# Kernel tuning notes

Measured on AMD Instinct MI355X. Metric: run time of the kernel, lower is better.

The kernel has to match this reference:

```python
import jax, jax.numpy as jnp
import numpy as np

TMP = 1.0  # temperature from init

def setup_inputs() -> dict:
    key = jax.random.key(0)
    k1, k2, k3 = jax.random.split(key, 3)
    B, D, C = 8192, 1024, 4096
    x = jax.random.normal(k1, (B, D), dtype=jnp.float32)
    mod = jax.random.normal(k2, (B, D), dtype=jnp.float32)
    W = jax.random.normal(k3, (C, D), dtype=jnp.float32) * 0.02  # cls.weight
    return {"x": x, "mod": mod, "W": W}

def reference(x, mod, W):
    # att = softmax(mod / tmp, axis=1) + 1, shape (B, D)
    att = jax.nn.softmax(mod / TMP, axis=1) + 1.0
    # result[b, c] = sum_d W[c, d] * att[b, d] * x[b, d]
    # == (att * x) @ W.T  -- collapses the repeat + per-sample matvec loop
    return jnp.einsum('bd,cd->bc', att * x, W)
```

## Files before the change

### kernel.cpp

```cpp
#include <hip/hip_runtime.h>
#include <hip/hip_bf16.h>
#include <cstdint>
#include <cstddef>

typedef __bf16 bf16_t;
typedef __bf16 bf16x8 __attribute__((ext_vector_type(8)));
typedef __bf16 bf16x4 __attribute__((ext_vector_type(4)));
typedef float  f32x4  __attribute__((ext_vector_type(4)));

#define KDIM 1024
#define NT   16

__global__ void prep_kernel(const float* __restrict__ x,
                            const float* __restrict__ mod,
                            const float* __restrict__ W,
                            bf16_t* __restrict__ a,
                            bf16_t* __restrict__ Wb,
                            int D, int Bn) {
  if ((int)blockIdx.x >= Bn) {
    const size_t i = (((size_t)blockIdx.x - Bn) * blockDim.x + threadIdx.x) * 8;
    float4 u = *(const float4*)(W + i);
    float4 v = *(const float4*)(W + i + 4);
    bf16x8 o;
    o[0] = (bf16_t)u.x; o[1] = (bf16_t)u.y; o[2] = (bf16_t)u.z; o[3] = (bf16_t)u.w;
    o[4] = (bf16_t)v.x; o[5] = (bf16_t)v.y; o[6] = (bf16_t)v.z; o[7] = (bf16_t)v.w;
    *(bf16x8*)(Wb + i) = o;
    return;
  }

  const int b = blockIdx.x;
  const int t = threadIdx.x;
  const size_t row = (size_t)b * D;

  float4 mv = ((const float4*)(mod + row))[t];
  float mx = fmaxf(fmaxf(mv.x, mv.y), fmaxf(mv.z, mv.w));
#pragma unroll
  for (int o = 32; o > 0; o >>= 1) mx = fmaxf(mx, __shfl_xor(mx, o));

  __shared__ float redmax[4];
  __shared__ float redsum[4];
  const int wave = t >> 6, lane = t & 63;
  if (lane == 0) redmax[wave] = mx;
  __syncthreads();
  mx = fmaxf(fmaxf(redmax[0], redmax[1]), fmaxf(redmax[2], redmax[3]));

  float4 e;
  e.x = __expf(mv.x - mx); e.y = __expf(mv.y - mx);
  e.z = __expf(mv.z - mx); e.w = __expf(mv.w - mx);
  float s = (e.x + e.y) + (e.z + e.w);
#pragma unroll
  for (int o = 32; o > 0; o >>= 1) s += __shfl_xor(s, o);
  if (lane == 0) redsum[wave] = s;
  __syncthreads();
  s = (redsum[0] + redsum[1]) + (redsum[2] + redsum[3]);

  const float inv = 1.0f / s;
  float4 xv = ((const float4*)(x + row))[t];
  bf16x4 o4;
  o4[0] = (bf16_t)((e.x * inv + 1.0f) * xv.x);
  o4[1] = (bf16_t)((e.y * inv + 1.0f) * xv.y);
  o4[2] = (bf16_t)((e.z * inv + 1.0f) * xv.z);
  o4[3] = (bf16_t)((e.w * inv + 1.0f) * xv.w);
  *((bf16x4*)(a + row) + t) = o4;
}

__global__ __launch_bounds__(512, 2) void gemm256_kernel(
    const bf16_t* __restrict__ A, const bf16_t* __restrict__ B,
    float* __restrict__ C, int M, int N) {
  __shared__ __align__(16) bf16_t lds[2 * 32768];

  const int tid  = threadIdx.x;
  const int wave = tid >> 6;
  const int lane = tid & 63;
  const int quad = lane >> 4;
  const int l16  = lane & 15;
  const int wm   = wave >> 2;
  const int wn   = wave & 3;

  const int nwg = gridDim.x;
  int flat = blockIdx.x;
  flat = (flat & 7) * (nwg >> 3) + (flat >> 3);
  const int ntiles = N >> 8;
  const int m0 = (flat / ntiles) << 8;
  const int n0 = (flat % ntiles) << 8;

  const int trow = tid >> 3;
  const int colg = (tid & 7) ^ (trow & 7);
  const bf16_t* aSrc = A + (size_t)(m0 + trow) * KDIM + colg * 8;
  const bf16_t* bSrc = B + (size_t)(n0 + trow) * KDIM + colg * 8;
  const int ldsW = wave * 512;

#define GLDS(src_, dst_) __builtin_amdgcn_global_load_lds( \
      (const __attribute__((address_space(1))) void*)(src_), \
      (__attribute__((address_space(3))) void*)(dst_), 16, 0, 0)

#define ISSUE_A(h, t_) do { \
      const bf16_t* s_ = aSrc + (size_t)((h) * 128) * KDIM + (t_) * 64; \
      bf16_t* d_ = lds + ((t_) & 1) * 32768 + (h) * 8192 + ldsW; \
      GLDS(s_, d_); \
      GLDS(s_ + (size_t)64 * KDIM, d_ + 4096); \
    } while (0)

#define ISSUE_B(h, t_) do { \
      const bf16_t* s_ = bSrc + (size_t)((h) * 128) * KDIM + (t_) * 64; \
      bf16_t* d_ = lds + ((t_) & 1) * 32768 + 16384 + (h) * 8192 + ldsW; \
      GLDS(s_, d_); \
      GLDS(s_ + (size_t)64 * KDIM, d_ + 4096); \
    } while (0)

  ISSUE_A(0, 0); ISSUE_A(1, 0);
  ISSUE_B(0, 0); ISSUE_B(1, 0);
  ISSUE_B(0, 1); ISSUE_B(1, 1);

  f32x4 acc[8][4];
#pragma unroll
  for (int i = 0; i < 8; ++i)
#pragma unroll
    for (int j = 0; j < 4; ++j) acc[i][j] = (f32x4){0.f, 0.f, 0.f, 0.f};

  const int aBase = (wm * 128 + l16) * 64;
  const int bBase = (wn * 64 + l16) * 64;
  const int c0 = ((quad)     ^ (l16 & 7)) * 8;
  const int c1 = ((4 + quad) ^ (l16 & 7)) * 8;

  asm volatile("s_waitcnt vmcnt(4)" ::: "memory");
  __builtin_amdgcn_s_barrier();

  bf16x8 bfr[4][2];
  bf16x8 afA[2][2], afB[2][2];

#define BPANEL(Bt_) do { \
      _Pragma("unroll") \
      for (int j = 0; j < 4; ++j) { \
        bfr[j][0] = *(const bf16x8*)((Bt_) + bBase + j * 16 * 64 + c0); \
        bfr[j][1] = *(const bf16x8*)((Bt_) + bBase + j * 16 * 64 + c1); \
      } \
    } while (0)

#define RD_AF(S_, q_) do { \
      _Pragma("unroll") \
      for (int i = 0; i < 2; ++i) { \
        S_[i][0] = *(const bf16x8*)(At + aBase + ((q_) * 32 + i * 16) * 64 + c0); \
        S_[i][1] = *(const bf16x8*)(At + aBase + ((q_) * 32 + i * 16) * 64 + c1); \
      } \
    } while (0)

#define MFMA16(q_, S_) do { \
      _Pragma("unroll") \
      for (int i = 0; i < 2; ++i) \
        _Pragma("unroll") \
        for (int j = 0; j < 4; ++j) { \
          acc[(q_) * 2 + i][j] = __builtin_amdgcn_mfma_f32_16x16x32_bf16( \
              S_[i][0], bfr[j][0], acc[(q_) * 2 + i][j], 0, 0, 0); \
          acc[(q_) * 2 + i][j] = __builtin_amdgcn_mfma_f32_16x16x32_bf16( \
              S_[i][1], bfr[j][1], acc[(q_) * 2 + i][j], 0, 0, 0); \
        } \
    } while (0)

#define PH(qcur_, SCUR_, SNXT_, qnxt_, ISSUE_STMT, LGKM_STR, END_STMT) do { \
      if ((qnxt_) >= 0) { RD_AF(SNXT_, ((qnxt_) & 3)); } \
      ISSUE_STMT; \
      asm volatile("" ::: "memory"); \
      __builtin_amdgcn_s_barrier(); \
      asm volatile(LGKM_STR ::: "memory"); \
      __builtin_amdgcn_sched_barrier(0); \
      __builtin_amdgcn_s_setprio(1); \
      MFMA16(qcur_, SCUR_); \
      __builtin_amdgcn_s_setprio(0); \
      END_STMT; \
      asm volatile("" ::: "memory"); \
      __builtin_amdgcn_s_barrier(); \
    } while (0)

#pragma unroll 1
  for (int t = 0; t < NT; ++t) {
    const bf16_t* At = lds + (t & 1) * 32768;
    const bf16_t* Bt = At + 16384;

    BPANEL(Bt);
    RD_AF(afA, 0);

    PH(0, afA, afB, 1, if (t + 1 < NT) ISSUE_A(0, t + 1),
       "s_waitcnt lgkmcnt(4)", (void)0);
    PH(1, afB, afA, 2, if (t + 1 < NT) ISSUE_A(1, t + 1),
       "s_waitcnt lgkmcnt(4)", (void)0);
    PH(2, afA, afB, 3, if (t + 2 < NT) ISSUE_B(0, t + 2),
       "s_waitcnt lgkmcnt(4)", (void)0);
    PH(3, afB, afA, -1, if (t + 2 < NT) ISSUE_B(1, t + 2),
       "s_waitcnt lgkmcnt(0)",
       if (t < NT - 2) { asm volatile("s_waitcnt vmcnt(4)" ::: "memory"); }
       else            { asm volatile("s_waitcnt vmcnt(0)" ::: "memory"); });
  }

#pragma unroll
  for (int ri = 0; ri < 8; ++ri) {
    const int mg = m0 + wm * 128 + ri * 16 + quad * 4;
#pragma unroll
    for (int j = 0; j < 4; ++j) {
      const int ng = n0 + wn * 64 + j * 16 + l16;
#pragma unroll
      for (int r = 0; r < 4; ++r)
        C[(size_t)(mg + r) * N + ng] = acc[ri][j][r];
    }
  }
}

extern "C" void kernel_launch(void* const* d_in, const int* in_sizes, int n_in,
                              void* d_out, int out_size, void* d_ws, size_t ws_size,
                              hipStream_t stream) {
  const float* x   = (const float*)d_in[0];
  const float* mod = (const float*)d_in[1];
  const float* W   = (const float*)d_in[2];
  float* out = (float*)d_out;

  const int D = 1024;
  const int Bn = in_sizes[0] / D;
  const int Cn = in_sizes[2] / D;

  bf16_t* a  = (bf16_t*)d_ws;
  bf16_t* Wb = (bf16_t*)((char*)d_ws + (size_t)Bn * D * sizeof(bf16_t));

  const int castBlocks = (Cn * D) / (256 * 8);
  prep_kernel<<<Bn + castBlocks, 256, 0, stream>>>(x, mod, W, a, Wb, D, Bn);

  const int nwg = (Bn / 256) * (Cn / 256);
  gemm256_kernel<<<nwg, 512, 0, stream>>>(a, Wb, out, Bn, Cn);
}
```

Measured before the change: 256.2 us.

## Load B fragments directly from global into registers, keep only A in LDS

The GEMM stops staging B tiles through LDS. Each wave now loads its B fragments straight from global memory into double-buffered registers two K-tiles ahead, and only A goes through LDS via global_load_lds. The K loop is also restructured into a simpler per-tile schedule with one barrier per tile instead of the four-phase interleaved pipeline. This halves LDS traffic and footprint, at the cost of more VGPRs, uncoalesced per-lane global loads of B, and redundant B loads across the wm waves.

New measurement: 278.1 us. +8.5%, slower.

```diff
diff --git a/kernel.cpp b/kernel.cpp
--- a/kernel.cpp
+++ b/kernel.cpp
@@ -67,7 +67,7 @@
 __global__ __launch_bounds__(512, 2) void gemm256_kernel(
     const bf16_t* __restrict__ A, const bf16_t* __restrict__ B,
     float* __restrict__ C, int M, int N) {
-  __shared__ __align__(16) bf16_t lds[2 * 32768];
+  __shared__ __align__(16) bf16_t As[2][16384];
 
   const int tid  = threadIdx.x;
   const int wave = tid >> 6;
@@ -87,30 +87,36 @@
   const int trow = tid >> 3;
   const int colg = (tid & 7) ^ (trow & 7);
   const bf16_t* aSrc = A + (size_t)(m0 + trow) * KDIM + colg * 8;
-  const bf16_t* bSrc = B + (size_t)(n0 + trow) * KDIM + colg * 8;
   const int ldsW = wave * 512;
 
 #define GLDS(src_, dst_) __builtin_amdgcn_global_load_lds( \
       (const __attribute__((address_space(1))) void*)(src_), \
       (__attribute__((address_space(3))) void*)(dst_), 16, 0, 0)
 
-#define ISSUE_A(h, t_) do { \
-      const bf16_t* s_ = aSrc + (size_t)((h) * 128) * KDIM + (t_) * 64; \
-      bf16_t* d_ = lds + ((t_) & 1) * 32768 + (h) * 8192 + ldsW; \
-      GLDS(s_, d_); \
-      GLDS(s_ + (size_t)64 * KDIM, d_ + 4096); \
-    } while (0)
-
-#define ISSUE_B(h, t_) do { \
-      const bf16_t* s_ = bSrc + (size_t)((h) * 128) * KDIM + (t_) * 64; \
-      bf16_t* d_ = lds + ((t_) & 1) * 32768 + 16384 + (h) * 8192 + ldsW; \
-      GLDS(s_, d_); \
-      GLDS(s_ + (size_t)64 * KDIM, d_ + 4096); \
-    } while (0)
-
-  ISSUE_A(0, 0); ISSUE_A(1, 0);
-  ISSUE_B(0, 0); ISSUE_B(1, 0);
-  ISSUE_B(0, 1); ISSUE_B(1, 1);
+#define STAGE_A(t_) do { \
+      if ((t_) < NT) { \
+        _Pragma("unroll") \
+        for (int i_ = 0; i_ < 4; ++i_) { \
+          GLDS(aSrc + (size_t)(i_ * 64) * KDIM + (t_) * 64, \
+               &As[(t_) & 1][i_ * 4096 + ldsW]); \
+        } \
+      } \
+    } while (0)
+
+  const bf16_t* bP[4];
+#pragma unroll
+  for (int j = 0; j < 4; ++j)
+    bP[j] = B + (size_t)(n0 + wn * 64 + j * 16 + l16) * KDIM + quad * 8;
+
+#define PRELOAD_B(DST_, t_) do { \
+      if ((t_) < NT) { \
+        _Pragma("unroll") \
+        for (int j_ = 0; j_ < 4; ++j_) { \
+          DST_[j_][0] = *(const bf16x8*)(bP[j_] + (t_) * 64); \
+          DST_[j_][1] = *(const bf16x8*)(bP[j_] + (t_) * 64 + 32); \
+        } \
+      } \
+    } while (0)
 
   f32x4 acc[8][4];
 #pragma unroll
@@ -119,77 +125,54 @@
     for (int j = 0; j < 4; ++j) acc[i][j] = (f32x4){0.f, 0.f, 0.f, 0.f};
 
   const int aBase = (wm * 128 + l16) * 64;
-  const int bBase = (wn * 64 + l16) * 64;
   const int c0 = ((quad)     ^ (l16 & 7)) * 8;
   const int c1 = ((4 + quad) ^ (l16 & 7)) * 8;
 
-  asm volatile("s_waitcnt vmcnt(4)" ::: "memory");
+  bf16x8 bX[4][2], bY[4][2];
+
+  STAGE_A(0);
+  PRELOAD_B(bX, 0);
+  PRELOAD_B(bY, 1);
+  asm volatile("s_waitcnt vmcnt(8)" ::: "memory");
   __builtin_amdgcn_s_barrier();
 
-  bf16x8 bfr[4][2];
-  bf16x8 afA[2][2], afB[2][2];
-
-#define BPANEL(Bt_) do { \
+#define MFMA16(q_, af_, BF_) do { \
       _Pragma("unroll") \
-      for (int j = 0; j < 4; ++j) { \
-        bfr[j][0] = *(const bf16x8*)((Bt_) + bBase + j * 16 * 64 + c0); \
-        bfr[j][1] = *(const bf16x8*)((Bt_) + bBase + j * 16 * 64 + c1); \
+      for (int i_ = 0; i_ < 2; ++i_) \
+        _Pragma("unroll") \
+        for (int j_ = 0; j_ < 4; ++j_) { \
+          acc[(q_) * 2 + i_][j_] = __builtin_amdgcn_mfma_f32_16x16x32_bf16( \
+              af_[i_][0], BF_[j_][0], acc[(q_) * 2 + i_][j_], 0, 0, 0); \
+          acc[(q_) * 2 + i_][j_] = __builtin_amdgcn_mfma_f32_16x16x32_bf16( \
+              af_[i_][1], BF_[j_][1], acc[(q_) * 2 + i_][j_], 0, 0, 0); \
+        } \
+    } while (0)
+
+#define TILE(t_, BCUR_, BNXT_) do { \
+      const bf16_t* At = As[(t_) & 1]; \
+      STAGE_A((t_) + 1); \
+      _Pragma("unroll") \
+      for (int q_ = 0; q_ < 4; ++q_) { \
+        bf16x8 af_[2][2]; \
+        _Pragma("unroll") \
+        for (int i_ = 0; i_ < 2; ++i_) { \
+          af_[i_][0] = *(const bf16x8*)(At + aBase + (q_ * 32 + i_ * 16) * 64 + c0); \
+          af_[i_][1] = *(const bf16x8*)(At + aBase + (q_ * 32 + i_ * 16) * 64 + c1); \
+        } \
+        __builtin_amdgcn_s_setprio(1); \
+        MFMA16(q_, af_, BCUR_); \
+        __builtin_amdgcn_s_setprio(0); \
       } \
-    } while (0)
-
-#define RD_AF(S_, q_) do { \
-      _Pragma("unroll") \
-      for (int i = 0; i < 2; ++i) { \
-        S_[i][0] = *(const bf16x8*)(At + aBase + ((q_) * 32 + i * 16) * 64 + c0); \
-        S_[i][1] = *(const bf16x8*)(At + aBase + ((q_) * 32 + i * 16) * 64 + c1); \
-      } \
-    } while (0)
-
-#define MFMA16(q_, S_) do { \
-      _Pragma("unroll") \
-      for (int i = 0; i < 2; ++i) \
-        _Pragma("unroll") \
-        for (int j = 0; j < 4; ++j) { \
-          acc[(q_) * 2 + i][j] = __builtin_amdgcn_mfma_f32_16x16x32_bf16( \
-              S_[i][0], bfr[j][0], acc[(q_) * 2 + i][j], 0, 0, 0); \
-          acc[(q_) * 2 + i][j] = __builtin_amdgcn_mfma_f32_16x16x32_bf16( \
-              S_[i][1], bfr[j][1], acc[(q_) * 2 + i][j], 0, 0, 0); \
-        } \
-    } while (0)
-
-#define PH(qcur_, SCUR_, SNXT_, qnxt_, ISSUE_STMT, LGKM_STR, END_STMT) do { \
-      if ((qnxt_) >= 0) { RD_AF(SNXT_, ((qnxt_) & 3)); } \
-      ISSUE_STMT; \
-      asm volatile("" ::: "memory"); \
+      PRELOAD_B(BNXT_, (t_) + 2); \
+      if ((t_) < NT - 2) { asm volatile("s_waitcnt vmcnt(8)" ::: "memory"); } \
+      else               { asm volatile("s_waitcnt vmcnt(0)" ::: "memory"); } \
       __builtin_amdgcn_s_barrier(); \
-      asm volatile(LGKM_STR ::: "memory"); \
-      __builtin_amdgcn_sched_barrier(0); \
-      __builtin_amdgcn_s_setprio(1); \
-      MFMA16(qcur_, SCUR_); \
-      __builtin_amdgcn_s_setprio(0); \
-      END_STMT; \
-      asm volatile("" ::: "memory"); \
-      __builtin_amdgcn_s_barrier(); \
     } while (0)
 
 #pragma unroll 1
-  for (int t = 0; t < NT; ++t) {
-    const bf16_t* At = lds + (t & 1) * 32768;
-    const bf16_t* Bt = At + 16384;
-
-    BPANEL(Bt);
-    RD_AF(afA, 0);
-
-    PH(0, afA, afB, 1, if (t + 1 < NT) ISSUE_A(0, t + 1),
-       "s_waitcnt lgkmcnt(4)", (void)0);
-    PH(1, afB, afA, 2, if (t + 1 < NT) ISSUE_A(1, t + 1),
-       "s_waitcnt lgkmcnt(4)", (void)0);
-    PH(2, afA, afB, 3, if (t + 2 < NT) ISSUE_B(0, t + 2),
-       "s_waitcnt lgkmcnt(4)", (void)0);
-    PH(3, afB, afA, -1, if (t + 2 < NT) ISSUE_B(1, t + 2),
-       "s_waitcnt lgkmcnt(0)",
-       if (t < NT - 2) { asm volatile("s_waitcnt vmcnt(4)" ::: "memory"); }
-       else            { asm volatile("s_waitcnt vmcnt(0)" ::: "memory"); });
+  for (int tt = 0; tt < NT; tt += 2) {
+    TILE(tt,     bX, bX);
+    TILE(tt + 1, bY, bY);
   }
 
 #pragma unroll
```
